# Performance work log

Hardware: AMD Instinct MI355X
Metric: run time of the kernel (lower is better)

## Reference

```python
import jax, jax.numpy as jnp
import numpy as np

HEAD_DIM = 128
NEG_INF = -1e10


def setup_inputs() -> dict:
    key = jax.random.key(0)
    k1, k2, k3, k4 = jax.random.split(key, 4)
    B, T, C, D = 4, 4096, 1024, HEAD_DIM
    x = jax.random.normal(k1, (B, T, C), dtype=jnp.float32)
    # nn.Linear(C, D, bias=False) weight is [D, C]; we store transposed [C, D]
    Wq = jax.random.normal(k2, (C, D), dtype=jnp.float32) * (1.0 / np.sqrt(C))
    Wk = jax.random.normal(k3, (C, D), dtype=jnp.float32) * (1.0 / np.sqrt(C))
    Wv = jax.random.normal(k4, (C, D), dtype=jnp.float32) * (1.0 / np.sqrt(C))
    return {"x": x, "Wq": Wq, "Wk": Wk, "Wv": Wv}


def reference(x, Wq, Wk, Wv):
    B, T, C = x.shape
    D = Wq.shape[1]
    Q = jnp.einsum("btc,cd->btd", x, Wq)
    K = jnp.einsum("btc,cd->btd", x, Wk)
    V = jnp.einsum("btc,cd->btd", x, Wv)
    scores = jnp.einsum("bqd,bkd->bqk", Q, K) * (1.0 / np.sqrt(D))
    causal = jnp.tril(jnp.ones((T, T), dtype=bool))  # [T, T]
    scores = jnp.where(causal, scores, NEG_INF)
    probs = jax.nn.softmax(scores, axis=-1)
    out = jnp.einsum("bqk,bkd->bqd", probs, V)
    return out
```

## Files before the change

### kernel.cpp

```cpp
#include <hip/hip_runtime.h>
#include <hip/hip_bf16.h>
#include <stdint.h>
#include <math.h>


typedef __attribute__((ext_vector_type(4))) float f32x4;
typedef __attribute__((ext_vector_type(8))) short bf16x8;
typedef __attribute__((ext_vector_type(4))) unsigned short u16x4;
typedef __attribute__((ext_vector_type(2))) unsigned int u32x2;

#define NBATCH 4
#define NT 4096
#define NC 1024
#define ND 128
#define BT (NBATCH * NT)
#define NSPLIT 8
#define KSPAN (NT / NSPLIT)

#define EXP2F(x) __builtin_amdgcn_exp2f(x)

__device__ __forceinline__ unsigned short f2bf(float f) {
  union { float f; uint32_t u; } v; v.f = f;
  uint32_t u = v.u;
  return (unsigned short)((u + 0x7FFFu + ((u >> 16) & 1u)) >> 16);
}

__device__ __forceinline__ float bf2f(unsigned short h) {
  union { uint32_t u; float f; } v; v.u = ((uint32_t)h) << 16;
  return v.f;
}

__device__ __forceinline__ bf16x8 cvt8(const f32x4 a0, const f32x4 a1) {
  bf16x8 r;
  r[0] = (short)f2bf(a0[0]); r[1] = (short)f2bf(a0[1]);
  r[2] = (short)f2bf(a0[2]); r[3] = (short)f2bf(a0[3]);
  r[4] = (short)f2bf(a1[0]); r[5] = (short)f2bf(a1[1]);
  r[6] = (short)f2bf(a1[2]); r[7] = (short)f2bf(a1[3]);
  return r;
}

__device__ __forceinline__ unsigned int cvtpk(float a, float b) {
  unsigned int r;
  asm("v_cvt_pk_bf16_f32 %0, %1, %2" : "=v"(r) : "v"(a), "v"(b));
  return r;
}

__device__ __forceinline__ void g2lds16(const void* g, void* l) {
  __builtin_amdgcn_global_load_lds(
      (const __attribute__((address_space(1))) unsigned int*)g,
      (__attribute__((address_space(3))) unsigned int*)l, 16, 0, 0);
}

__global__ void wcvt_kernel(const float* __restrict__ Wq, const float* __restrict__ Wk,
                            const float* __restrict__ Wv, unsigned short* __restrict__ Wt) {
  const float CK = 0.12751744f;
  int idx = blockIdx.x * blockDim.x + threadIdx.x;
  int m = idx >> 17;
  int r = idx & 131071;
  int d = r >> 10;
  int c = r & 1023;
  const float* W = (m == 0) ? Wq : (m == 1) ? Wk : Wv;
  float v = W[c * ND + d];
  if (m == 1) v *= CK;
  Wt[idx] = f2bf(v);
}

__global__ __launch_bounds__(256, 3)
void proj_kernel(const float* __restrict__ x, const unsigned short* __restrict__ Wt,
                 unsigned short* __restrict__ Qb, unsigned short* __restrict__ Kb,
                 unsigned short* __restrict__ Vt) {
  __shared__ char smem[2][16384];

  int w = threadIdx.x >> 6;
  int lane = threadIdx.x & 63;
  int r16 = lane & 15;
  int h4 = lane >> 4;
  int wm = w & 1;
  int wn = w >> 1;

  int mt = blockIdx.x & 255;
  int nt = blockIdx.x >> 8;

  const char* xg = (const char*)(x + (size_t)(mt * 64) * NC);
  const char* wg = (const char*)(Wt + (size_t)(nt * 128) * NC);

  f32x4 acc[2][4];
  #pragma unroll
  for (int m = 0; m < 2; ++m)
    #pragma unroll
    for (int n = 0; n < 4; ++n) acc[m][n] = (f32x4){0.f, 0.f, 0.f, 0.f};

  int cA0 = (w * 2 + 0) * 64 + lane;
  int cA1 = (w * 2 + 1) * 64 + lane;

  #define STAGE(buf, t)                                                          \
    {                                                                            \
      int c0 = (t) * 32;                                                         \
      {                                                                          \
        int c = cA0, row = c >> 3, s = c & 7;                                    \
        g2lds16(xg + (size_t)row * 4096 + c0 * 4 + ((s ^ (row & 7)) << 4),       \
                smem[buf] + (w * 2 + 0) * 1024);                                 \
      }                                                                          \
      {                                                                          \
        int c = cA1, row = c >> 3, s = c & 7;                                    \
        g2lds16(xg + (size_t)row * 4096 + c0 * 4 + ((s ^ (row & 7)) << 4),       \
                smem[buf] + (w * 2 + 1) * 1024);                                 \
      }                                                                          \
      {                                                                          \
        int c = cA0, row = c >> 2, s = c & 3;                                    \
        g2lds16(wg + (size_t)row * 2048 + c0 * 2 + ((s ^ (row & 3)) << 4),       \
                smem[buf] + 8192 + (w * 2 + 0) * 1024);                          \
      }                                                                          \
      {                                                                          \
        int c = cA1, row = c >> 2, s = c & 3;                                    \
        g2lds16(wg + (size_t)row * 2048 + c0 * 2 + ((s ^ (row & 3)) << 4),       \
                smem[buf] + 8192 + (w * 2 + 1) * 1024);                          \
      }                                                                          \
    }

  STAGE(0, 0);
  __syncthreads();

  for (int t = 0; t < 32; ++t) {
    int cur = t & 1;
    if (t + 1 < 32) STAGE(cur ^ 1, t + 1);

    bf16x8 af[2];
    #pragma unroll
    for (int m = 0; m < 2; ++m) {
      int row = wm * 32 + m * 16 + r16;
      f32x4 a0 = *(const f32x4*)(smem[cur] + row * 128 + (((h4 * 2) ^ (row & 7)) << 4));
      f32x4 a1 = *(const f32x4*)(smem[cur] + row * 128 + (((h4 * 2 + 1) ^ (row & 7)) << 4));
      af[m] = cvt8(a0, a1);
    }
    __builtin_amdgcn_s_setprio(1);
    #pragma unroll
    for (int n = 0; n < 4; ++n) {
      int brow = wn * 64 + n * 16 + r16;
      bf16x8 bfr = *(const bf16x8*)(smem[cur] + 8192 + brow * 64 + ((h4 ^ (brow & 3)) << 4));
      acc[0][n] = __builtin_amdgcn_mfma_f32_16x16x32_bf16(af[0], bfr, acc[0][n], 0, 0, 0);
      acc[1][n] = __builtin_amdgcn_mfma_f32_16x16x32_bf16(af[1], bfr, acc[1][n], 0, 0, 0);
    }
    __builtin_amdgcn_s_setprio(0);
    __syncthreads();
  }
  #undef STAGE

  if (nt < 2) {
    unsigned short* dst = (nt == 0) ? Qb : Kb;
    #pragma unroll
    for (int m = 0; m < 2; ++m) {
      int t0 = mt * 64 + wm * 32 + m * 16 + h4 * 4;
      #pragma unroll
      for (int n = 0; n < 4; ++n) {
        int d = wn * 64 + n * 16 + r16;
        #pragma unroll
        for (int r = 0; r < 4; ++r)
          dst[(size_t)(t0 + r) * ND + d] = f2bf(acc[m][n][r]);
      }
    }
  } else {
    #pragma unroll
    for (int m = 0; m < 2; ++m) {
      int t0 = mt * 64 + wm * 32 + m * 16 + h4 * 4;
      int b = t0 >> 12;
      int tl = t0 & (NT - 1);
      #pragma unroll
      for (int n = 0; n < 4; ++n) {
        int d = wn * 64 + n * 16 + r16;
        u16x4 pk;
        #pragma unroll
        for (int r = 0; r < 4; ++r) pk[r] = f2bf(acc[m][n][r]);
        *(u16x4*)(Vt + (size_t)b * (ND * NT) + (size_t)d * NT + tl) = pk;
      }
    }
  }
}

__global__ __launch_bounds__(256, 2)
void attn_kernel(const unsigned short* __restrict__ Qb,
                 const unsigned short* __restrict__ Kb,
                 const unsigned short* __restrict__ Vt,
                 unsigned short* __restrict__ Opart, float* __restrict__ Mpart,
                 float* __restrict__ Lpart) {
  __shared__ unsigned short kbuf[64 * 128];
  __shared__ unsigned short vbuf[128 * 64];
  __shared__ unsigned short plds[4][32][72];

  int wave = threadIdx.x >> 6;
  int lane = threadIdx.x & 63;
  int r16 = lane & 15;
  int h4 = lane >> 4;
  int h8 = h4 * 8;

  int l = blockIdx.x;
  int b = l & 3;
  int u = l >> 2;
  int a = (int)((sqrtf(2.0f * (float)u + 1.0f) - 1.0f) * 0.5f);
  if (a < 0) a = 0;
  while (2 * (a + 1) * (a + 2) <= u) ++a;
  while (a > 0 && 2 * a * (a + 1) > u) --a;
  int rem = u - 2 * a * (a + 1);
  int apl = a + 1;
  int rr = rem / apl;
  int s = rem - rr * apl;
  int qbt = 4 * a + rr;

  int qb0 = qbt * 128;
  int z = s;
  int kstart = s << 9;
  int kend = min(qb0 + 128, kstart + KSPAN);

  int q0 = qb0 + wave * 32;

  const unsigned short* Qbb = Qb + (size_t)b * NT * ND;
  const unsigned short* Kbb = Kb + (size_t)b * NT * ND;
  const unsigned short* Vtb = Vt + (size_t)b * ND * NT;

  bf16x8 qf[2][4];
  #pragma unroll
  for (int f = 0; f < 2; ++f)
    #pragma unroll
    for (int dc = 0; dc < 4; ++dc)
      qf[f][dc] = *(const bf16x8*)(Qbb + (size_t)(q0 + f * 16 + r16) * ND + dc * 32 + h8);

  f32x4 accO[2][8];
  #pragma unroll
  for (int f = 0; f < 2; ++f)
    #pragma unroll
    for (int i = 0; i < 8; ++i) accO[f][i] = (f32x4){0.f, 0.f, 0.f, 0.f};
  float mr[2] = {-1e30f, -1e30f};
  float lr[2] = {0.f, 0.f};

  for (int kv0 = kstart; kv0 < kend; kv0 += 64) {
    #pragma unroll
    for (int i = 0; i < 4; ++i) {
      int e = i * 256 + wave * 64 + lane;
      int krow = e >> 4, ks = e & 15;
      const char* gk = (const char*)(Kbb + (size_t)(kv0 + krow) * ND)
                       + ((ks * 16) ^ ((krow & 7) << 4));
      g2lds16(gk, (char*)kbuf + (size_t)(i * 256 + wave * 64) * 16);
    }
    #pragma unroll
    for (int i = 0; i < 4; ++i) {
      int e = i * 256 + wave * 64 + lane;
      int vrow = e >> 3, vs = e & 7;
      const char* gv = (const char*)(Vtb + (size_t)vrow * NT + kv0)
                       + ((vs * 16) ^ ((vrow & 7) << 4));
      g2lds16(gv, (char*)vbuf + (size_t)(i * 256 + wave * 64) * 16);
    }
    __syncthreads();

    if (kv0 < q0 + 32) {
      f32x4 sT[2][4];
      __builtin_amdgcn_s_setprio(1);
      #pragma unroll
      for (int kt = 0; kt < 4; ++kt) {
        sT[0][kt] = (f32x4){0.f, 0.f, 0.f, 0.f};
        sT[1][kt] = (f32x4){0.f, 0.f, 0.f, 0.f};
        int krow = kt * 16 + r16;
        #pragma unroll
        for (int dc = 0; dc < 4; ++dc) {
          int off = krow * 256 + ((dc * 64 + h4 * 16) ^ ((krow & 7) << 4));
          bf16x8 kf = *(const bf16x8*)((const char*)kbuf + off);
          sT[0][kt] = __builtin_amdgcn_mfma_f32_16x16x32_bf16(kf, qf[0][dc], sT[0][kt], 0, 0, 0);
          sT[1][kt] = __builtin_amdgcn_mfma_f32_16x16x32_bf16(kf, qf[1][dc], sT[1][kt], 0, 0, 0);
        }
      }
      __builtin_amdgcn_s_setprio(0);

      float pmax[2] = {-3e38f, -3e38f};
      if (kv0 + 63 <= q0) {
        #pragma unroll
        for (int kt = 0; kt < 4; ++kt)
          #pragma unroll
          for (int f = 0; f < 2; ++f)
            #pragma unroll
            for (int r = 0; r < 4; ++r) pmax[f] = fmaxf(pmax[f], sT[f][kt][r]);
      } else {
        #pragma unroll
        for (int kt = 0; kt < 4; ++kt) {
          int kb = kv0 + kt * 16 + h4 * 4;
          #pragma unroll
          for (int f = 0; f < 2; ++f) {
            int q = q0 + f * 16 + r16;
            #pragma unroll
            for (int r = 0; r < 4; ++r) {
              float v = (kb + r <= q) ? sT[f][kt][r] : -3e38f;
              sT[f][kt][r] = v;
              pmax[f] = fmaxf(pmax[f], v);
            }
          }
        }
      }

      bool grow = (pmax[0] > mr[0] + 11.0f) || (pmax[1] > mr[1] + 11.0f);
      if (__any(grow)) {
        float sf[2], sfa[2][4];
        #pragma unroll
        for (int f = 0; f < 2; ++f) {
          pmax[f] = fmaxf(pmax[f], __shfl_xor(pmax[f], 16, 64));
          pmax[f] = fmaxf(pmax[f], __shfl_xor(pmax[f], 32, 64));
          float mn = fmaxf(mr[f], pmax[f]);
          sf[f] = EXP2F(mr[f] - mn);
          mr[f] = mn;
          lr[f] *= sf[f];
        }
        #pragma unroll
        for (int f = 0; f < 2; ++f)
          #pragma unroll
          for (int r = 0; r < 4; ++r) sfa[f][r] = __shfl(sf[f], h4 * 4 + r, 64);
        #pragma unroll
        for (int f = 0; f < 2; ++f)
          #pragma unroll
          for (int dt = 0; dt < 8; ++dt) {
            #pragma unroll
            for (int r = 0; r < 4; ++r) accO[f][dt][r] *= sfa[f][r];
          }
      }

      #pragma unroll
      for (int f = 0; f < 2; ++f) {
        #pragma unroll
        for (int kt = 0; kt < 4; ++kt) {
          float p0 = EXP2F(sT[f][kt][0] - mr[f]);
          float p1 = EXP2F(sT[f][kt][1] - mr[f]);
          float p2 = EXP2F(sT[f][kt][2] - mr[f]);
          float p3 = EXP2F(sT[f][kt][3] - mr[f]);
          lr[f] += (p0 + p1) + (p2 + p3);
          u32x2 pk;
          pk[0] = cvtpk(p0, p1);
          pk[1] = cvtpk(p2, p3);
          *(u32x2*)&plds[wave][f * 16 + r16][kt * 16 + h4 * 4] = pk;
        }
      }

      __builtin_amdgcn_s_setprio(1);
      #pragma unroll
      for (int kc = 0; kc < 2; ++kc) {
        bf16x8 pf0 = *(const bf16x8*)(&plds[wave][r16][kc * 32 + h8]);
        bf16x8 pf1 = *(const bf16x8*)(&plds[wave][16 + r16][kc * 32 + h8]);
        #pragma unroll
        for (int dt = 0; dt < 8; ++dt) {
          int vrow = dt * 16 + r16;
          int off = vrow * 128 + ((kc * 64 + h4 * 16) ^ ((vrow & 7) << 4));
          bf16x8 vf = *(const bf16x8*)((const char*)vbuf + off);
          accO[0][dt] = __builtin_amdgcn_mfma_f32_16x16x32_bf16(pf0, vf, accO[0][dt], 0, 0, 0);
          accO[1][dt] = __builtin_amdgcn_mfma_f32_16x16x32_bf16(pf1, vf, accO[1][dt], 0, 0, 0);
        }
      }
      __builtin_amdgcn_s_setprio(0);
    }
    __syncthreads();
  }

  #pragma unroll
  for (int f = 0; f < 2; ++f) {
    lr[f] += __shfl_xor(lr[f], 16, 64);
    lr[f] += __shfl_xor(lr[f], 32, 64);
  }

  size_t pbase = ((size_t)z * NBATCH + b) * NT + q0;
  #pragma unroll
  for (int f = 0; f < 2; ++f)
    #pragma unroll
    for (int dt = 0; dt < 8; ++dt)
      #pragma unroll
      for (int r = 0; r < 4; ++r)
        Opart[(pbase + f * 16 + h4 * 4 + r) * ND + dt * 16 + r16] = f2bf(accO[f][dt][r]);
  if (h4 == 0) {
    #pragma unroll
    for (int f = 0; f < 2; ++f) {
      Mpart[pbase + f * 16 + r16] = mr[f];
      Lpart[pbase + f * 16 + r16] = lr[f];
    }
  }
}

__global__ void merge_kernel(const unsigned short* __restrict__ Opart,
                             const float* __restrict__ Mpart,
                             const float* __restrict__ Lpart, float* __restrict__ out) {
  int idx = blockIdx.x * blockDim.x + threadIdx.x;
  int bq = idx >> 4;
  int dg = idx & 15;
  int q = bq & (NT - 1);
  int nz = (q >> 9) + 1;

  float M = -3e38f;
  #pragma unroll
  for (int zz = 0; zz < NSPLIT; ++zz)
    if (zz < nz) M = fmaxf(M, Mpart[(size_t)zz * BT + bq]);

  float denom = 0.f;
  float o[8] = {0.f, 0.f, 0.f, 0.f, 0.f, 0.f, 0.f, 0.f};
  #pragma unroll
  for (int zz = 0; zz < NSPLIT; ++zz) {
    if (zz < nz) {
      float e = EXP2F(Mpart[(size_t)zz * BT + bq] - M);
      denom += e * Lpart[(size_t)zz * BT + bq];
      bf16x8 ov = *(const bf16x8*)(Opart + ((size_t)zz * BT + bq) * ND + dg * 8);
      #pragma unroll
      for (int j = 0; j < 8; ++j) o[j] += e * bf2f((unsigned short)ov[j]);
    }
  }
  float inv = 1.0f / denom;
  f32x4 o0, o1;
  #pragma unroll
  for (int j = 0; j < 4; ++j) { o0[j] = o[j] * inv; o1[j] = o[4 + j] * inv; }
  float* dst = out + (size_t)bq * ND + dg * 8;
  *(f32x4*)dst = o0;
  *(f32x4*)(dst + 4) = o1;
}

extern "C" void kernel_launch(void* const* d_in, const int* in_sizes, int n_in,
                              void* d_out, int out_size, void* d_ws, size_t ws_size,
                              hipStream_t stream) {
  const float* x  = (const float*)d_in[0];
  const float* Wq = (const float*)d_in[1];
  const float* Wk = (const float*)d_in[2];
  const float* Wv = (const float*)d_in[3];

  char* ws = (char*)d_ws;
  unsigned short* Qb = (unsigned short*)ws;
  unsigned short* Kb = (unsigned short*)(ws + 4194304);
  unsigned short* Vt = (unsigned short*)(ws + 8388608);
  unsigned short* Opart = (unsigned short*)(ws + 12582912);
  float* Mpart = (float*)(ws + 46137344);
  float* Lpart = (float*)(ws + 46661632);
  unsigned short* Wt = (unsigned short*)(ws + 12582912);

  hipLaunchKernelGGL(wcvt_kernel, dim3(1536), dim3(256), 0, stream, Wq, Wk, Wv, Wt);
  hipLaunchKernelGGL(proj_kernel, dim3(768), dim3(256), 0, stream, x, Wt, Qb, Kb, Vt);
  hipLaunchKernelGGL(attn_kernel, dim3(576), dim3(256), 0, stream,
                     Qb, Kb, Vt, Opart, Mpart, Lpart);
  hipLaunchKernelGGL(merge_kernel, dim3(BT * 16 / 256), dim3(256), 0, stream,
                     Opart, Mpart, Lpart, (float*)d_out);
}
```

Before: 79.74 us.

## Retune LDS swizzles, packed bf16 conversion, and attention occupancy bound

Swaps the scalar float-to-bf16 rounding in the projection GEMM for packed v_cvt_pk_bf16_f32 conversions. It also changes the weight-tile LDS swizzle to XOR on row>>1 to reduce bank conflicts. In the attention kernel, the padded P staging buffer becomes an XOR-swizzled unpadded layout, the K/V LDS destination addressing is simplified, and launch bounds are raised to 3 blocks per CU. The higher occupancy target may force register spills given the large accumulator arrays.

Result: no change. 79.72 us (-0.0%).

```diff
diff --git a/kernel.cpp b/kernel.cpp
--- a/kernel.cpp
+++ b/kernel.cpp
@@ -30,19 +30,19 @@
   return v.f;
 }
 
-__device__ __forceinline__ bf16x8 cvt8(const f32x4 a0, const f32x4 a1) {
-  bf16x8 r;
-  r[0] = (short)f2bf(a0[0]); r[1] = (short)f2bf(a0[1]);
-  r[2] = (short)f2bf(a0[2]); r[3] = (short)f2bf(a0[3]);
-  r[4] = (short)f2bf(a1[0]); r[5] = (short)f2bf(a1[1]);
-  r[6] = (short)f2bf(a1[2]); r[7] = (short)f2bf(a1[3]);
-  return r;
-}
-
 __device__ __forceinline__ unsigned int cvtpk(float a, float b) {
   unsigned int r;
   asm("v_cvt_pk_bf16_f32 %0, %1, %2" : "=v"(r) : "v"(a), "v"(b));
   return r;
+}
+
+__device__ __forceinline__ bf16x8 cvt8pk(const f32x4 a0, const f32x4 a1) {
+  union { unsigned int u[4]; bf16x8 v; } r;
+  r.u[0] = cvtpk(a0[0], a0[1]);
+  r.u[1] = cvtpk(a0[2], a0[3]);
+  r.u[2] = cvtpk(a1[0], a1[1]);
+  r.u[3] = cvtpk(a1[2], a1[3]);
+  return r.v;
 }
 
 __device__ __forceinline__ void g2lds16(const void* g, void* l) {
@@ -108,12 +108,12 @@
       }                                                                          \
       {                                                                          \
         int c = cA0, row = c >> 2, s = c & 3;                                    \
-        g2lds16(wg + (size_t)row * 2048 + c0 * 2 + ((s ^ (row & 3)) << 4),       \
+        g2lds16(wg + (size_t)row * 2048 + c0 * 2 + ((s ^ ((row >> 1) & 3)) << 4),\
                 smem[buf] + 8192 + (w * 2 + 0) * 1024);                          \
       }                                                                          \
       {                                                                          \
         int c = cA1, row = c >> 2, s = c & 3;                                    \
-        g2lds16(wg + (size_t)row * 2048 + c0 * 2 + ((s ^ (row & 3)) << 4),       \
+        g2lds16(wg + (size_t)row * 2048 + c0 * 2 + ((s ^ ((row >> 1) & 3)) << 4),\
                 smem[buf] + 8192 + (w * 2 + 1) * 1024);                          \
       }                                                                          \
     }
@@ -131,13 +131,14 @@
       int row = wm * 32 + m * 16 + r16;
       f32x4 a0 = *(const f32x4*)(smem[cur] + row * 128 + (((h4 * 2) ^ (row & 7)) << 4));
       f32x4 a1 = *(const f32x4*)(smem[cur] + row * 128 + (((h4 * 2 + 1) ^ (row & 7)) << 4));
-      af[m] = cvt8(a0, a1);
+      af[m] = cvt8pk(a0, a1);
     }
     __builtin_amdgcn_s_setprio(1);
     #pragma unroll
     for (int n = 0; n < 4; ++n) {
       int brow = wn * 64 + n * 16 + r16;
-      bf16x8 bfr = *(const bf16x8*)(smem[cur] + 8192 + brow * 64 + ((h4 ^ (brow & 3)) << 4));
+      bf16x8 bfr = *(const bf16x8*)(smem[cur] + 8192 + brow * 64 +
+                                    ((h4 ^ ((brow >> 1) & 3)) << 4));
       acc[0][n] = __builtin_amdgcn_mfma_f32_16x16x32_bf16(af[0], bfr, acc[0][n], 0, 0, 0);
       acc[1][n] = __builtin_amdgcn_mfma_f32_16x16x32_bf16(af[1], bfr, acc[1][n], 0, 0, 0);
     }
@@ -177,7 +178,7 @@
   }
 }
 
-__global__ __launch_bounds__(256, 2)
+__global__ __launch_bounds__(256, 3)
 void attn_kernel(const unsigned short* __restrict__ Qb,
                  const unsigned short* __restrict__ Kb,
                  const unsigned short* __restrict__ Vt,
@@ -185,13 +186,14 @@
                  float* __restrict__ Lpart) {
   __shared__ unsigned short kbuf[64 * 128];
   __shared__ unsigned short vbuf[128 * 64];
-  __shared__ unsigned short plds[4][32][72];
+  __shared__ unsigned short plds[4][2048];
 
   int wave = threadIdx.x >> 6;
   int lane = threadIdx.x & 63;
   int r16 = lane & 15;
   int h4 = lane >> 4;
   int h8 = h4 * 8;
+  int a7 = r16 & 7;
 
   int l = blockIdx.x;
   int b = l & 3;
@@ -239,7 +241,7 @@
       int krow = e >> 4, ks = e & 15;
       const char* gk = (const char*)(Kbb + (size_t)(kv0 + krow) * ND)
                        + ((ks * 16) ^ ((krow & 7) << 4));
-      g2lds16(gk, (char*)kbuf + (size_t)(i * 256 + wave * 64) * 16);
+      g2lds16(gk, (char*)kbuf + (size_t)e * 16);
     }
     #pragma unroll
     for (int i = 0; i < 4; ++i) {
@@ -247,7 +249,7 @@
       int vrow = e >> 3, vs = e & 7;
       const char* gv = (const char*)(Vtb + (size_t)vrow * NT + kv0)
                        + ((vs * 16) ^ ((vrow & 7) << 4));
-      g2lds16(gv, (char*)vbuf + (size_t)(i * 256 + wave * 64) * 16);
+      g2lds16(gv, (char*)vbuf + (size_t)e * 16);
     }
     __syncthreads();
 
@@ -321,6 +323,7 @@
 
       #pragma unroll
       for (int f = 0; f < 2; ++f) {
+        int row = f * 16 + r16;
         #pragma unroll
         for (int kt = 0; kt < 4; ++kt) {
           float p0 = EXP2F(sT[f][kt][0] - mr[f]);
@@ -331,15 +334,17 @@
           u32x2 pk;
           pk[0] = cvtpk(p0, p1);
           pk[1] = cvtpk(p2, p3);
-          *(u32x2*)&plds[wave][f * 16 + r16][kt * 16 + h4 * 4] = pk;
+          int slot = (2 * kt + (h4 >> 1)) ^ a7;
+          *(u32x2*)&plds[wave][row * 64 + slot * 8 + (h4 & 1) * 4] = pk;
         }
       }
 
       __builtin_amdgcn_s_setprio(1);
       #pragma unroll
       for (int kc = 0; kc < 2; ++kc) {
-        bf16x8 pf0 = *(const bf16x8*)(&plds[wave][r16][kc * 32 + h8]);
-        bf16x8 pf1 = *(const bf16x8*)(&plds[wave][16 + r16][kc * 32 + h8]);
+        int sl = ((4 * kc + h4) ^ a7) * 8;
+        bf16x8 pf0 = *(const bf16x8*)(&plds[wave][r16 * 64 + sl]);
+        bf16x8 pf1 = *(const bf16x8*)(&plds[wave][(16 + r16) * 64 + sl]);
         #pragma unroll
         for (int dt = 0; dt < 8; ++dt) {
           int vrow = dt * 16 + r16;
```
